# Performance work log

Measured on AMD Instinct MI355X. Metric: run time of the kernel, lower is better.

The kernel has to match this reference:

```python
import jax, jax.numpy as jnp
import numpy as np

B, N, H = 8, 2000, 64  # batch, num_nodes(=input_dim), hidden(num_gru_units)


def _laplacian_self_loop(a):
    # batched: norm = D^{-1/2} (A + I) D^{-1/2}
    m = a + jnp.eye(a.shape[-1], dtype=a.dtype)
    d_inv_sqrt = jnp.sum(m, axis=-1) ** -0.5  # (B, N)
    return d_inv_sqrt[..., :, None] * m * d_inv_sqrt[..., None, :]


def _graph_conv(inputs, hidden_flat, adj, windd, W2, b2, W3, b3, W, b, out_dim):
    b_, _, n = inputs.shape
    # dynamic wind-based adjacency
    wind_now = inputs[:, 2, :] * 360.0  # (B, N)
    direction = jnp.abs(windd[None, :, :] - wind_now[:, :, None])  # (B, N, N)
    direction = jnp.where(direction > 360.0, 180.0, direction)
    d1 = jnp.maximum(jnp.cos(direction * (jnp.pi / 180.0)), 0.0)
    a = d1 @ W2.T + b2 + (adj @ W3.T + b3)[None]  # (B, N, N)
    a1 = _laplacian_self_loop(jnp.maximum(a, 0.0))
    # graph conv: concat [x, h] then A @ [.] then Linear
    x = jnp.concatenate([inputs[:, 0, :, None], hidden_flat.reshape(b_, n, H)], axis=2)  # (B,N,H+1)
    y = jnp.einsum('bij,bjh->bih', a1, x) @ W.T + b  # (B, N, out_dim)
    return y.reshape(b_, n * out_dim)


def reference(inputs, hidden_state, adj, windd, W2, b2, W3, b3, W1a, b1a, W1b, b1b, Wca1, Wca2, Wsa):
    b_, _, n = inputs.shape
    conc = _graph_conv(inputs, hidden_state, adj, windd, W2, b2, W3, b3, W1a, b1a, 2 * H)
    conc = conc.reshape(b_, 2 * H, n)  # faithful reshape (input_dim == N)
    # --- channel attention (CBAM) ---
    avg = jnp.mean(conc, axis=2, keepdims=True)  # (B, 2H, 1)
    mx = jnp.max(conc, axis=2, keepdims=True)
    def fc(v):
        return jnp.einsum('oc,bcx->box', Wca2, jax.nn.relu(jnp.einsum('oc,bcx->box', Wca1, v)))
    ca = jax.nn.sigmoid(fc(avg) + fc(mx))  # (B, 2H, 1)
    conc = ca * conc
    # --- spatial attention ---
    s = jnp.stack([jnp.mean(conc, axis=1), jnp.max(conc, axis=1)], axis=1)  # (B, 2, N)
    sa = jax.lax.conv_general_dilated(s, Wsa, window_strides=(1,), padding=((3, 3),),
                                      dimension_numbers=('NCH', 'OIH', 'NCH'))  # (B,1,N)
    conc = jax.nn.sigmoid(sa) * conc
    # --- GRU gates ---
    conc = jax.nn.sigmoid(conc.reshape(b_, 2 * H * n))
    r, u = jnp.split(conc, 2, axis=1)  # each (B, N*H)
    c = jnp.tanh(_graph_conv(inputs, r * hidden_state, adj, windd, W2, b2, W3, b3, W1b, b1b, H))
    new_hidden_state = u * hidden_state + (1.0 - u) * c
    return new_hidden_state


def setup_inputs() -> dict:
    key = jax.random.key(0)
    ks = jax.random.split(key, 12)
    inputs = jax.random.uniform(ks[0], (B, 3, N), dtype=jnp.float32)
    hidden_state = jax.random.normal(ks[1], (B, N * H), dtype=jnp.float32) * 0.1
    adj = jax.random.uniform(ks[2], (N, N), dtype=jnp.float32)
    windd = jax.random.uniform(ks[3], (N, N), dtype=jnp.float32) * 360.0
    sN = 1.0 / np.sqrt(N)
    W2 = jax.random.normal(ks[4], (N, N), dtype=jnp.float32) * sN
    b2 = jnp.zeros((N,), jnp.float32)
    W3 = jax.random.normal(ks[5], (N, N), dtype=jnp.float32) * sN
    b3 = jnp.zeros((N,), jnp.float32)
    sI = 1.0 / np.sqrt(H + 1)
    W1a = jax.random.normal(ks[6], (2 * H, H + 1), dtype=jnp.float32) * sI
    b1a = jnp.ones((2 * H,), jnp.float32)  # bias=1.0 in graph_conv1
    W1b = jax.random.normal(ks[7], (H, H + 1), dtype=jnp.float32) * sI
    b1b = jnp.zeros((H,), jnp.float32)
    Wca1 = jax.random.normal(ks[8], (2 * H // 16, 2 * H), dtype=jnp.float32) * (1.0 / np.sqrt(2 * H))
    Wca2 = jax.random.normal(ks[9], (2 * H, 2 * H // 16), dtype=jnp.float32) * (1.0 / np.sqrt(2 * H // 16))
    Wsa = jax.random.normal(ks[10], (1, 2, 7), dtype=jnp.float32) * (1.0 / np.sqrt(14))
    return {'inputs': inputs, 'hidden_state': hidden_state, 'adj': adj, 'windd': windd,
            'W2': W2, 'b2': b2, 'W3': W3, 'b3': b3, 'W1a': W1a, 'b1a': b1a,
            'W1b': W1b, 'b1b': b1b, 'Wca1': Wca1, 'Wca2': Wca2, 'Wsa': Wsa}
```

## Files before the change

### kernel.cpp

```cpp
#include <hip/hip_runtime.h>

#define NN 2000
#define BB 8
#define P  2048
#define NIT 32

typedef __attribute__((ext_vector_type(8))) short bf16x8;
typedef __attribute__((ext_vector_type(4))) float f32x4;

__device__ __forceinline__ float sigf(float x) { return 1.0f / (1.0f + expf(-x)); }

__device__ __forceinline__ short f2bf(float x) {
    union { float f; unsigned u; } v; v.f = x;
    unsigned r = v.u + 0x7fffu + ((v.u >> 16) & 1u);
    return (short)(r >> 16);
}
__device__ __forceinline__ float bf2f(short h) {
    union { unsigned u; float f; } v; v.u = ((unsigned)(unsigned short)h) << 16; return v.f;
}

__device__ __forceinline__ void gl2lds16(const short* g, short* l) {
    __builtin_amdgcn_global_load_lds(
        (const __attribute__((address_space(1))) void*)g,
        (__attribute__((address_space(3))) void*)l, 16, 0, 0);
}

__global__ __launch_bounds__(256) void k_cvtW(
    const float* __restrict__ s0, const float* __restrict__ s1, const float* __restrict__ s2,
    short* __restrict__ d0, short* __restrict__ d1, short* __restrict__ d2)
{
    const int i = blockIdx.x, sel = blockIdx.y, t = threadIdx.x;
    const float* s = (sel == 0) ? s0 : (sel == 1) ? s1 : s2;
    short* d = ((sel == 0) ? d0 : (sel == 1) ? d1 : d2) + ((size_t)i) * P + t * 8;
    bf16x8 v;
#pragma unroll
    for (int e = 0; e < 8; ++e) v[e] = 0;
    if (i < NN && t < 250) {
        const float* p = s + (size_t)i * NN + t * 8;
        float4 x0 = *(const float4*)p;
        float4 x1 = *(const float4*)(p + 4);
        float a[8] = {x0.x,x0.y,x0.z,x0.w,x1.x,x1.y,x1.z,x1.w};
#pragma unroll
        for (int e = 0; e < 8; ++e) v[e] = f2bf(a[e]);
    }
    *(bf16x8*)d = v;
}

__global__ __launch_bounds__(256) void k_cvtD1(
    const float* __restrict__ windd, const float* __restrict__ inputs, short* __restrict__ d1bf)
{
    const int i = blockIdx.x, t = threadIdx.x;
    const bool live = (i < NN) && (t < 250);
    float a[8];
    if (live) {
        const float* p = windd + (size_t)i * NN + t * 8;
        float4 x0 = *(const float4*)p;
        float4 x1 = *(const float4*)(p + 4);
        a[0]=x0.x; a[1]=x0.y; a[2]=x0.z; a[3]=x0.w;
        a[4]=x1.x; a[5]=x1.y; a[6]=x1.z; a[7]=x1.w;
    }
#pragma unroll
    for (int b = 0; b < BB; ++b) {
        bf16x8 v;
#pragma unroll
        for (int e = 0; e < 8; ++e) v[e] = 0;
        if (live) {
            const float wn = inputs[(size_t)b * 3 * NN + 2 * NN + i] * 360.0f;
#pragma unroll
            for (int e = 0; e < 8; ++e) {
                float dd = fabsf(a[e] - wn);
                dd = (dd > 360.0f) ? 180.0f : dd;
                float c = __cosf(dd * 0.01745329251994329577f);
                v[e] = f2bf(fmaxf(c, 0.0f));
            }
        }
        *(bf16x8*)(d1bf + ((size_t)b * P + i) * P + t * 8) = v;
    }
}

__global__ __launch_bounds__(512, 2) void k_gd(
    const short* __restrict__ d1bf, const short* __restrict__ W2bf,
    const float* __restrict__ b2, const short* __restrict__ adjw,
    short* __restrict__ m_bf)
{
    __shared__ char smem[131072];
    const int t = threadIdx.x;
    const int w = t >> 6, lane = t & 63;
    const int wm = w >> 2, wn = w & 3;
    const int lr = lane & 15, lq = lane >> 4;
    const int tile = blockIdx.x;
    const int b = blockIdx.y;
    const int i0 = (tile & 7) * 256;
    const int j0 = (tile >> 3) * 256;
    const short* A  = d1bf + (size_t)b * P * P;
    const short* Bm = W2bf;

    const short* srcA[4];
    const short* srcB[4];
#pragma unroll
    for (int q = 0; q < 4; ++q) {
        const int c = q * 512 + t;
        const int r = c >> 3;
        const int g = (c & 7) ^ (r & 7);
        srcA[q] = A  + (size_t)(i0 + r) * P + g * 8;
        srcB[q] = Bm + (size_t)(j0 + r) * P + g * 8;
    }

#define STAGE_A(slot, ktI) do {                                                        \
        gl2lds16(srcA[0] + (ktI) * 64, (short*)(smem + (slot) * 32768 + (w * 64) * 16));          \
        gl2lds16(srcA[1] + (ktI) * 64, (short*)(smem + (slot) * 32768 + (512 + w * 64) * 16));    \
        gl2lds16(srcA[2] + (ktI) * 64, (short*)(smem + (slot) * 32768 + (1024 + w * 64) * 16));   \
        gl2lds16(srcA[3] + (ktI) * 64, (short*)(smem + (slot) * 32768 + (1536 + w * 64) * 16)); } while (0)
#define STAGE_B(slot, ktI) do {                                                        \
        gl2lds16(srcB[0] + (ktI) * 64, (short*)(smem + 65536 + (slot) * 32768 + (w * 64) * 16));          \
        gl2lds16(srcB[1] + (ktI) * 64, (short*)(smem + 65536 + (slot) * 32768 + (512 + w * 64) * 16));    \
        gl2lds16(srcB[2] + (ktI) * 64, (short*)(smem + 65536 + (slot) * 32768 + (1024 + w * 64) * 16));   \
        gl2lds16(srcB[3] + (ktI) * 64, (short*)(smem + 65536 + (slot) * 32768 + (1536 + w * 64) * 16)); } while (0)

    const int fx0 = (lq << 4) ^ ((lr & 7) << 4);
    const int fx1 = ((4 + lq) << 4) ^ ((lr & 7) << 4);
    const int arowB = (wm * 128 + lr) * 128;
    const int browB = (wn * 64 + lr) * 128;

    f32x4 acc[8][4];
#pragma unroll
    for (int m = 0; m < 8; ++m)
#pragma unroll
        for (int n = 0; n < 4; ++n) acc[m][n] = (f32x4){0.f, 0.f, 0.f, 0.f};
    bf16x8 aF[4][2], bF[4][2];

    STAGE_A(0, 0);
    STAGE_B(0, 0);
    asm volatile("s_waitcnt vmcnt(0)" ::: "memory");
    __builtin_amdgcn_s_barrier();
    asm volatile("" ::: "memory");

#define MFMA_(a_, b_, m, n) acc[m][n] = __builtin_amdgcn_mfma_f32_16x16x32_bf16(a_, b_, acc[m][n], 0, 0, 0)

    for (int kt = 0; kt < NIT; ++kt) {
        char* curA = smem + (kt & 1) * 32768;
        char* curB = smem + 65536 + (kt & 1) * 32768;
        const int stgSlot = (kt + 1) & 1;
        const int stgKt = (kt + 1 < NIT) ? (kt + 1) : (NIT - 1);

#pragma unroll
        for (int m = 0; m < 4; ++m) {
            aF[m][0] = *(const bf16x8*)(curA + arowB + m * 2048 + fx0);
            aF[m][1] = *(const bf16x8*)(curA + arowB + m * 2048 + fx1);
        }
#pragma unroll
        for (int n = 0; n < 4; ++n) {
            bF[n][0] = *(const bf16x8*)(curB + browB + n * 2048 + fx0);
            bF[n][1] = *(const bf16x8*)(curB + browB + n * 2048 + fx1);
        }
        STAGE_A(stgSlot, stgKt);
        asm volatile("s_waitcnt lgkmcnt(0)" ::: "memory");
        __builtin_amdgcn_sched_barrier(0);
        __builtin_amdgcn_s_setprio(1);
#pragma unroll
        for (int m = 0; m < 4; ++m)
#pragma unroll
            for (int n = 0; n < 4; ++n) {
                MFMA_(aF[m][0], bF[n][0], m, n);
                MFMA_(aF[m][1], bF[n][1], m, n);
            }
        __builtin_amdgcn_s_setprio(0);

#pragma unroll
        for (int m = 0; m < 4; ++m) {
            aF[m][0] = *(const bf16x8*)(curA + arowB + (m + 4) * 2048 + fx0);
            aF[m][1] = *(const bf16x8*)(curA + arowB + (m + 4) * 2048 + fx1);
        }
        STAGE_B(stgSlot, stgKt);
        asm volatile("s_waitcnt lgkmcnt(0)" ::: "memory");
        __builtin_amdgcn_sched_barrier(0);
        __builtin_amdgcn_s_setprio(1);
#pragma unroll
        for (int m = 0; m < 4; ++m)
#pragma unroll
            for (int n = 0; n < 4; ++n) {
                MFMA_(aF[m][0], bF[n][0], m + 4, n);
                MFMA_(aF[m][1], bF[n][1], m + 4, n);
            }
        __builtin_amdgcn_s_setprio(0);

        asm volatile("s_waitcnt vmcnt(0)" ::: "memory");
        __builtin_amdgcn_s_barrier();
        asm volatile("" ::: "memory");
    }

    const int rbase = i0 + wm * 128 + lq * 4;
    const int cbase = j0 + wn * 64 + lr;
#pragma unroll
    for (int m = 0; m < 8; ++m) {
#pragma unroll
        for (int n = 0; n < 4; ++n) {
            const int col = cbase + n * 16;
#pragma unroll
            for (int q = 0; q < 4; ++q) {
                const int row = rbase + m * 16 + q;
                short o = 0;
                if (row < NN && col < NN) {
                    float x = acc[m][n][q] + b2[col] + bf2f(adjw[(size_t)row * NN + col]);
                    x = fmaxf(x, 0.0f);
                    if (row == col) x += 1.0f;
                    o = f2bf(x);
                }
                m_bf[((size_t)b * P + row) * P + col] = o;
            }
        }
    }
#undef MFMA_
#undef STAGE_A
#undef STAGE_B
}

template<int EPI, int OUTD>
__global__ __launch_bounds__(256) void k_mfma(
    const short* __restrict__ Abase, const short* __restrict__ Bbase,
    const float* __restrict__ bias, const short* __restrict__ adjw,
    void* __restrict__ Cout, float* __restrict__ part, size_t aBatch)
{
    __shared__ short shA[4096];
    __shared__ short shB[4096];
    const int t = threadIdx.x;
    const int w = t >> 6, lane = t & 63;
    const int wr = w >> 1, wc = w & 1;

    int i0, j0, b, kt = 0;
    if (EPI == 2) {
        i0 = blockIdx.x * 128; j0 = 0; kt = blockIdx.y; b = blockIdx.z;
    } else {
        i0 = blockIdx.x * 128; j0 = blockIdx.y * 128; b = 0;
    }
    const int kb = (EPI == 2) ? kt * (P / 4) : 0;
    const int ke = (EPI == 2) ? kt * (P / 4) + (P / 4) : P;

    const short* A  = Abase + (size_t)b * aBatch;
    const short* Bm = Bbase + ((EPI == 2) ? (size_t)b * 128 * P : (size_t)0);

    f32x4 acc[4][4];
#pragma unroll
    for (int m = 0; m < 4; ++m)
#pragma unroll
        for (int n = 0; n < 4; ++n) acc[m][n] = (f32x4){0.f, 0.f, 0.f, 0.f};

    const int lidx0 = w * 128 + lane;
    const int lidx1 = lidx0 + 64;
    const short* aS0 = A  + (size_t)(i0 + (lidx0 >> 2)) * P + (lidx0 & 3) * 8;
    const short* aS1 = A  + (size_t)(i0 + (lidx1 >> 2)) * P + (lidx1 & 3) * 8;
    const short* bS0 = Bm + (size_t)(j0 + (lidx0 >> 2)) * P + (lidx0 & 3) * 8;
    const short* bS1 = Bm + (size_t)(j0 + (lidx1 >> 2)) * P + (lidx1 & 3) * 8;
    short* ldA0 = shA + (w * 128) * 8;
    short* ldA1 = shA + (w * 128 + 64) * 8;
    short* ldB0 = shB + (w * 128) * 8;
    short* ldB1 = shB + (w * 128 + 64) * 8;

    const int lr = lane & 15, lq = lane >> 4;
    const int aoff = (wr * 64 + lr) * 32 + lq * 8;
    const int boff = (wc * 64 + lr) * 32 + lq * 8;

    for (int k0 = kb; k0 < ke; k0 += 32) {
        gl2lds16(aS0 + k0, ldA0);
        gl2lds16(aS1 + k0, ldA1);
        gl2lds16(bS0 + k0, ldB0);
        gl2lds16(bS1 + k0, ldB1);
        __syncthreads();
        bf16x8 aF[4], bF[4];
#pragma unroll
        for (int m = 0; m < 4; ++m) aF[m] = *(const bf16x8*)(shA + aoff + m * 512);
#pragma unroll
        for (int n = 0; n < 4; ++n) bF[n] = *(const bf16x8*)(shB + boff + n * 512);
#pragma unroll
        for (int m = 0; m < 4; ++m)
#pragma unroll
            for (int n = 0; n < 4; ++n)
                acc[m][n] = __builtin_amdgcn_mfma_f32_16x16x32_bf16(aF[m], bF[n], acc[m][n], 0, 0, 0);
        __syncthreads();
    }

    const int rbase = i0 + wr * 64 + lq * 4;
    const int cbase = j0 + wc * 64 + lr;
#pragma unroll
    for (int m = 0; m < 4; ++m) {
#pragma unroll
        for (int n = 0; n < 4; ++n) {
            const int col = cbase + n * 16;
#pragma unroll
            for (int q = 0; q < 4; ++q) {
                const int row = rbase + m * 16 + q;
                float v = acc[m][n][q];
                if (EPI == 0) {
                    if (row < NN && col < NN)
                        ((short*)Cout)[(size_t)row * NN + col] = f2bf(v + bias[col]);
                } else {
                    if (row < NN && col < OUTD)
                        part[((size_t)(kt * BB + b) * NN + row) * OUTD + col] = v;
                }
            }
        }
    }
}

template<int OUTD>
__global__ __launch_bounds__(256) void k_comb(
    const float* __restrict__ part, const float* __restrict__ dinv,
    const float* __restrict__ bias, float* __restrict__ out)
{
    const size_t idx = (size_t)blockIdx.x * 256 + threadIdx.x;
    const size_t S = (size_t)BB * NN * OUTD;
    if (idx >= S) return;
    const int o = (int)(idx % OUTD);
    const size_t r = idx / OUTD;
    const int i = (int)(r % NN);
    const int b = (int)(r / NN);
    float s = ((part[idx] + part[idx + S]) + (part[idx + 2 * S] + part[idx + 3 * S]));
    out[idx] = s * dinv[b * NN + i] + bias[o];
}

__global__ __launch_bounds__(256) void k_rowsum_bf(const short* __restrict__ m_bf, float* __restrict__ dinv)
{
    const int i = blockIdx.x, b = blockIdx.y;
    const short* p = m_bf + ((size_t)b * P + i) * P + threadIdx.x * 8;
    bf16x8 v = *(const bf16x8*)p;
    float s = 0.0f;
#pragma unroll
    for (int e = 0; e < 8; ++e) s += bf2f(v[e]);
#pragma unroll
    for (int off = 32; off > 0; off >>= 1) s += __shfl_down(s, off);
    __shared__ float red[4];
    if ((threadIdx.x & 63) == 0) red[threadIdx.x >> 6] = s;
    __syncthreads();
    if (threadIdx.x == 0) dinv[b * NN + i] = rsqrtf(red[0] + red[1] + red[2] + red[3]);
}

template<int OUT>
__global__ __launch_bounds__(128) void k_xwT(
    const float* __restrict__ inputs, const float* __restrict__ hsrc,
    const float* __restrict__ W, const float* __restrict__ dinv, short* __restrict__ zT)
{
    const int b = blockIdx.y;
    const int j0 = blockIdx.x * 16;
    const int t = threadIdx.x;
    __shared__ float wl[128 * 65];
    __shared__ float xs[16 * 66];
    __shared__ float dj[16];
    for (int idx = t; idx < OUT * 65; idx += 128) wl[idx] = W[idx];
    for (int idx = t; idx < 16 * 64; idx += 128) {
        int jj = idx >> 6, hh = idx & 63, j = j0 + jj;
        xs[jj * 66 + 1 + hh] = (j < NN) ? hsrc[((size_t)b * NN + j) * 64 + hh] : 0.0f;
    }
    if (t < 16) {
        int j = j0 + t;
        xs[t * 66] = (j < NN) ? inputs[(size_t)b * 3 * NN + j] : 0.0f;
        dj[t] = (j < NN) ? dinv[b * NN + j] : 0.0f;
    }
    __syncthreads();
    for (int jj = 0; jj < 16; ++jj) {
        float a = 0.0f;
        if (t < OUT) {
            const float* xr = &xs[jj * 66];
            const float* wr = &wl[t * 65];
#pragma unroll
            for (int c = 0; c < 65; ++c) a = fmaf(xr[c], wr[c], a);
        }
        int j = j0 + jj;
        zT[((size_t)b * 128 + t) * P + j] = (t < OUT && j < NN) ? f2bf(a * dj[jj]) : (short)0;
    }
}

__global__ __launch_bounds__(256) void k_chred(const float* __restrict__ conc,
                                               float* __restrict__ avg, float* __restrict__ mx)
{
    const int bc = blockIdx.x;
    const float* p = conc + (size_t)bc * NN;
    float s = 0.0f, mv = -3.402823466e+38f;
    for (int n = threadIdx.x; n < NN; n += 256) { float v = p[n]; s += v; mv = fmaxf(mv, v); }
#pragma unroll
    for (int off = 32; off > 0; off >>= 1) {
        s += __shfl_down(s, off);
        mv = fmaxf(mv, __shfl_down(mv, off));
    }
    __shared__ float rs[4], rm[4];
    if ((threadIdx.x & 63) == 0) { rs[threadIdx.x >> 6] = s; rm[threadIdx.x >> 6] = mv; }
    __syncthreads();
    if (threadIdx.x == 0) {
        avg[bc] = (rs[0] + rs[1] + rs[2] + rs[3]) * (1.0f / NN);
        mx[bc]  = fmaxf(fmaxf(rm[0], rm[1]), fmaxf(rm[2], rm[3]));
    }
}

__global__ __launch_bounds__(128) void k_ca(
    const float* __restrict__ avg, const float* __restrict__ mx,
    const float* __restrict__ Wca1, const float* __restrict__ Wca2, float* __restrict__ ca)
{
    const int b = blockIdx.x, t = threadIdx.x;
    __shared__ float av[128], mv[128], h[16];
    av[t] = avg[b * 128 + t];
    mv[t] = mx[b * 128 + t];
    __syncthreads();
    if (t < 16) {
        int o8 = t & 7;
        const float* src = (t < 8) ? av : mv;
        float s = 0.0f;
        for (int c = 0; c < 128; ++c) s = fmaf(Wca1[o8 * 128 + c], src[c], s);
        h[t] = fmaxf(s, 0.0f);
    }
    __syncthreads();
    float s = 0.0f;
#pragma unroll
    for (int k = 0; k < 8; ++k) s = fmaf(Wca2[t * 8 + k], h[k] + h[8 + k], s);
    ca[b * 128 + t] = sigf(s);
}

__global__ __launch_bounds__(256) void k_satgate(
    const float* __restrict__ conc, const float* __restrict__ ca,
    const float* __restrict__ Wsa, const float* __restrict__ hidden,
    float* __restrict__ rh, float* __restrict__ u)
{
    const int b = blockIdx.y;
    const int n0 = blockIdx.x * 256;
    const int t = threadIdx.x;
    __shared__ float cas[128];
    __shared__ float wsa[14];
    __shared__ float s0l[262], s1l[262];
    if (t < 128) cas[t] = ca[b * 128 + t];
    if (t >= 128 && t < 142) wsa[t - 128] = Wsa[t - 128];
    __syncthreads();

    const float* cb = conc + (size_t)b * NN * 128;
    {
        const int n = n0 + t;
        float sm = 0.0f, sx = -3.402823466e+38f;
        if (n < NN) {
            for (int c = 0; c < 128; ++c) {
                float v = cas[c] * cb[(size_t)c * NN + n];
                sm += v; sx = fmaxf(sx, v);
            }
            s0l[t + 3] = sm * (1.0f / 128.0f);
            s1l[t + 3] = sx;
        } else { s0l[t + 3] = 0.0f; s1l[t + 3] = 0.0f; }
    }
    if (t < 6) {
        const int hn = (t < 3) ? (n0 - 3 + t) : (n0 + 256 + (t - 3));
        const int hi = (t < 3) ? t : (256 + t);
        float sm = 0.0f, sx = -3.402823466e+38f;
        if (hn >= 0 && hn < NN) {
            for (int c = 0; c < 128; ++c) {
                float v = cas[c] * cb[(size_t)c * NN + hn];
                sm += v; sx = fmaxf(sx, v);
            }
            s0l[hi] = sm * (1.0f / 128.0f);
            s1l[hi] = sx;
        } else { s0l[hi] = 0.0f; s1l[hi] = 0.0f; }
    }
    __syncthreads();

    const int n = n0 + t;
    if (n >= NN) return;
    float sa = 0.0f;
#pragma unroll
    for (int k = 0; k < 7; ++k)
        sa += wsa[k] * s0l[t + k] + wsa[7 + k] * s1l[t + k];
    float gs = sigf(sa);
    for (int c = 0; c < 128; ++c) {
        float v = gs * cas[c] * cb[(size_t)c * NN + n];
        float g = sigf(v);
        if (c < 64)
            rh[(size_t)b * NN * 64 + (size_t)c * NN + n] =
                g * hidden[(size_t)b * NN * 64 + (size_t)c * NN + n];
        else
            u[(size_t)b * NN * 64 + (size_t)(c - 64) * NN + n] = g;
    }
}

__global__ __launch_bounds__(256) void k_fin(
    const float* __restrict__ u, const float* __restrict__ hidden,
    const float* __restrict__ cpre, float* __restrict__ out)
{
    const size_t idx = (size_t)blockIdx.x * 256 + threadIdx.x;
    if (idx >= (size_t)BB * NN * 64) return;
    float uu = u[idx];
    out[idx] = uu * hidden[idx] + (1.0f - uu) * tanhf(cpre[idx]);
}

extern "C" void kernel_launch(void* const* d_in, const int* in_sizes, int n_in,
                              void* d_out, int out_size, void* d_ws, size_t ws_size,
                              hipStream_t stream)
{
    (void)in_sizes; (void)n_in; (void)out_size; (void)ws_size;
    const float* inputs = (const float*)d_in[0];
    const float* hidden = (const float*)d_in[1];
    const float* adj    = (const float*)d_in[2];
    const float* windd  = (const float*)d_in[3];
    const float* W2     = (const float*)d_in[4];
    const float* b2     = (const float*)d_in[5];
    const float* W3     = (const float*)d_in[6];
    const float* b3     = (const float*)d_in[7];
    const float* W1a    = (const float*)d_in[8];
    const float* b1a    = (const float*)d_in[9];
    const float* W1b    = (const float*)d_in[10];
    const float* b1b    = (const float*)d_in[11];
    const float* Wca1   = (const float*)d_in[12];
    const float* Wca2   = (const float*)d_in[13];
    const float* Wsa    = (const float*)d_in[14];
    float* out = (float*)d_out;

    char* W = (char*)d_ws;
    short* adjW3bf = (short*)(W + 0);
    short* W2bf    = (short*)(W + 8000000);
    short* W3bf    = (short*)(W + 16388608);
    short* adjbf   = (short*)(W + 24777216);
    short* m_bf    = (short*)(W + 16388608);
    char* D = W + 83497472;
    short* d1bf = (short*)D;
    float* dinv = (float*)(D + 0);
    float* avgb = (float*)(D + 64000);
    float* mxb  = (float*)(D + 68096);
    float* cab  = (float*)(D + 72192);
    short* zT   = (short*)(D + 204800);
    float* conc = (float*)(D + 4399104);
    float* rh   = (float*)(D + 12591104);
    float* ubuf = (float*)(D + 16687104);
    float* cpre = (float*)(D + 20783104);
    float* part = (float*)(D + 24879104);

    const size_t PP = (size_t)P * P;

    k_cvtW<<<dim3(P, 3), 256, 0, stream>>>(W2, W3, adj, W2bf, W3bf, adjbf);
    k_cvtD1<<<P, 256, 0, stream>>>(windd, inputs, d1bf);
    k_mfma<0, 0><<<dim3(16, 16, 1), 256, 0, stream>>>(adjbf, W3bf, b3, nullptr, adjW3bf, nullptr, 0);
    k_gd<<<dim3(64, BB), 512, 0, stream>>>(d1bf, W2bf, b2, adjW3bf, m_bf);
    k_rowsum_bf<<<dim3(NN, BB), 256, 0, stream>>>(m_bf, dinv);
    k_xwT<128><<<dim3(128, BB), 128, 0, stream>>>(inputs, hidden, W1a, dinv, zT);
    k_mfma<2, 128><<<dim3(16, 4, BB), 256, 0, stream>>>(m_bf, zT, nullptr, nullptr, nullptr, part, PP);
    k_comb<128><<<(BB * NN * 128 + 255) / 256, 256, 0, stream>>>(part, dinv, b1a, conc);
    k_chred<<<BB * 128, 256, 0, stream>>>(conc, avgb, mxb);
    k_ca<<<BB, 128, 0, stream>>>(avgb, mxb, Wca1, Wca2, cab);
    k_satgate<<<dim3(8, BB), 256, 0, stream>>>(conc, cab, Wsa, hidden, rh, ubuf);
    k_xwT<64><<<dim3(128, BB), 128, 0, stream>>>(inputs, rh, W1b, dinv, zT);
    k_mfma<2, 64><<<dim3(16, 4, BB), 256, 0, stream>>>(m_bf, zT, nullptr, nullptr, nullptr, part, PP);
    k_comb<64><<<(BB * NN * 64 + 255) / 256, 256, 0, stream>>>(part, dinv, b1b, cpre);
    k_fin<<<(BB * NN * 64 + 255) / 256, 256, 0, stream>>>(ubuf, hidden, cpre, out);
}
```

Baseline: 420.0 us.

## Issue all prefetch at loop top, store split-K partials as bf16, fuse final combine

The big GEMM kernel now issues the global-to-LDS prefetch for both A and B at the start of each k-iteration instead of interleaving it between the two MFMA halves. Split-K partial sums are written in bf16 rather than fp32, which halves that traffic but adds rounding error to the partials. The last combine kernel and the GRU final-blend kernel are merged into one, removing the cpre intermediate buffer and one launch.

```diff
diff --git a/kernel.cpp b/kernel.cpp
--- a/kernel.cpp
+++ b/kernel.cpp
@@ -106,12 +106,11 @@
         srcB[q] = Bm + (size_t)(j0 + r) * P + g * 8;
     }
 
-#define STAGE_A(slot, ktI) do {                                                        \
+#define STAGE_ALL(slot, ktI) do {                                                      \
         gl2lds16(srcA[0] + (ktI) * 64, (short*)(smem + (slot) * 32768 + (w * 64) * 16));          \
         gl2lds16(srcA[1] + (ktI) * 64, (short*)(smem + (slot) * 32768 + (512 + w * 64) * 16));    \
         gl2lds16(srcA[2] + (ktI) * 64, (short*)(smem + (slot) * 32768 + (1024 + w * 64) * 16));   \
-        gl2lds16(srcA[3] + (ktI) * 64, (short*)(smem + (slot) * 32768 + (1536 + w * 64) * 16)); } while (0)
-#define STAGE_B(slot, ktI) do {                                                        \
+        gl2lds16(srcA[3] + (ktI) * 64, (short*)(smem + (slot) * 32768 + (1536 + w * 64) * 16));   \
         gl2lds16(srcB[0] + (ktI) * 64, (short*)(smem + 65536 + (slot) * 32768 + (w * 64) * 16));          \
         gl2lds16(srcB[1] + (ktI) * 64, (short*)(smem + 65536 + (slot) * 32768 + (512 + w * 64) * 16));    \
         gl2lds16(srcB[2] + (ktI) * 64, (short*)(smem + 65536 + (slot) * 32768 + (1024 + w * 64) * 16));   \
@@ -129,8 +128,7 @@
         for (int n = 0; n < 4; ++n) acc[m][n] = (f32x4){0.f, 0.f, 0.f, 0.f};
     bf16x8 aF[4][2], bF[4][2];
 
-    STAGE_A(0, 0);
-    STAGE_B(0, 0);
+    STAGE_ALL(0, 0);
     asm volatile("s_waitcnt vmcnt(0)" ::: "memory");
     __builtin_amdgcn_s_barrier();
     asm volatile("" ::: "memory");
@@ -143,6 +141,8 @@
         const int stgSlot = (kt + 1) & 1;
         const int stgKt = (kt + 1 < NIT) ? (kt + 1) : (NIT - 1);
 
+        STAGE_ALL(stgSlot, stgKt);
+
 #pragma unroll
         for (int m = 0; m < 4; ++m) {
             aF[m][0] = *(const bf16x8*)(curA + arowB + m * 2048 + fx0);
@@ -153,7 +153,6 @@
             bF[n][0] = *(const bf16x8*)(curB + browB + n * 2048 + fx0);
             bF[n][1] = *(const bf16x8*)(curB + browB + n * 2048 + fx1);
         }
-        STAGE_A(stgSlot, stgKt);
         asm volatile("s_waitcnt lgkmcnt(0)" ::: "memory");
         __builtin_amdgcn_sched_barrier(0);
         __builtin_amdgcn_s_setprio(1);
@@ -171,7 +170,6 @@
             aF[m][0] = *(const bf16x8*)(curA + arowB + (m + 4) * 2048 + fx0);
             aF[m][1] = *(const bf16x8*)(curA + arowB + (m + 4) * 2048 + fx1);
         }
-        STAGE_B(stgSlot, stgKt);
         asm volatile("s_waitcnt lgkmcnt(0)" ::: "memory");
         __builtin_amdgcn_sched_barrier(0);
         __builtin_amdgcn_s_setprio(1);
@@ -211,15 +209,14 @@
         }
     }
 #undef MFMA_
-#undef STAGE_A
-#undef STAGE_B
+#undef STAGE_ALL
 }
 
 template<int EPI, int OUTD>
 __global__ __launch_bounds__(256) void k_mfma(
     const short* __restrict__ Abase, const short* __restrict__ Bbase,
     const float* __restrict__ bias, const short* __restrict__ adjw,
-    void* __restrict__ Cout, float* __restrict__ part, size_t aBatch)
+    void* __restrict__ Cout, short* __restrict__ part, size_t aBatch)
 {
     __shared__ short shA[4096];
     __shared__ short shB[4096];
@@ -295,7 +292,7 @@
                         ((short*)Cout)[(size_t)row * NN + col] = f2bf(v + bias[col]);
                 } else {
                     if (row < NN && col < OUTD)
-                        part[((size_t)(kt * BB + b) * NN + row) * OUTD + col] = v;
+                        part[((size_t)(kt * BB + b) * NN + row) * OUTD + col] = f2bf(v);
                 }
             }
         }
@@ -304,7 +301,7 @@
 
 template<int OUTD>
 __global__ __launch_bounds__(256) void k_comb(
-    const float* __restrict__ part, const float* __restrict__ dinv,
+    const short* __restrict__ part, const float* __restrict__ dinv,
     const float* __restrict__ bias, float* __restrict__ out)
 {
     const size_t idx = (size_t)blockIdx.x * 256 + threadIdx.x;
@@ -314,8 +311,28 @@
     const size_t r = idx / OUTD;
     const int i = (int)(r % NN);
     const int b = (int)(r / NN);
-    float s = ((part[idx] + part[idx + S]) + (part[idx + 2 * S] + part[idx + 3 * S]));
+    float s = (bf2f(part[idx]) + bf2f(part[idx + S])) +
+              (bf2f(part[idx + 2 * S]) + bf2f(part[idx + 3 * S]));
     out[idx] = s * dinv[b * NN + i] + bias[o];
+}
+
+__global__ __launch_bounds__(256) void k_cfin(
+    const short* __restrict__ part, const float* __restrict__ dinv,
+    const float* __restrict__ bias, const float* __restrict__ u,
+    const float* __restrict__ hidden, float* __restrict__ out)
+{
+    const size_t idx = (size_t)blockIdx.x * 256 + threadIdx.x;
+    const size_t S = (size_t)BB * NN * 64;
+    if (idx >= S) return;
+    const int o = (int)(idx & 63);
+    const size_t r = idx >> 6;
+    const int i = (int)(r % NN);
+    const int b = (int)(r / NN);
+    float s = (bf2f(part[idx]) + bf2f(part[idx + S])) +
+              (bf2f(part[idx + 2 * S]) + bf2f(part[idx + 3 * S]));
+    float c = tanhf(s * dinv[b * NN + i] + bias[o]);
+    float uu = u[idx];
+    out[idx] = uu * hidden[idx] + (1.0f - uu) * c;
 }
 
 __global__ __launch_bounds__(256) void k_rowsum_bf(const short* __restrict__ m_bf, float* __restrict__ dinv)
@@ -472,16 +489,6 @@
         else
             u[(size_t)b * NN * 64 + (size_t)(c - 64) * NN + n] = g;
     }
-}
-
-__global__ __launch_bounds__(256) void k_fin(
-    const float* __restrict__ u, const float* __restrict__ hidden,
-    const float* __restrict__ cpre, float* __restrict__ out)
-{
-    const size_t idx = (size_t)blockIdx.x * 256 + threadIdx.x;
-    if (idx >= (size_t)BB * NN * 64) return;
-    float uu = u[idx];
-    out[idx] = uu * hidden[idx] + (1.0f - uu) * tanhf(cpre[idx]);
 }
 
 extern "C" void kernel_launch(void* const* d_in, const int* in_sizes, int n_in,
@@ -522,8 +529,7 @@
     float* conc = (float*)(D + 4399104);
     float* rh   = (float*)(D + 12591104);
     float* ubuf = (float*)(D + 16687104);
-    float* cpre = (float*)(D + 20783104);
-    float* part = (float*)(D + 24879104);
+    short* part = (short*)(D + 24879104);
 
     const size_t PP = (size_t)P * P;
 
@@ -540,6 +546,5 @@
     k_satgate<<<dim3(8, BB), 256, 0, stream>>>(conc, cab, Wsa, hidden, rh, ubuf);
     k_xwT<64><<<dim3(128, BB), 128, 0, stream>>>(inputs, rh, W1b, dinv, zT);
     k_mfma<2, 64><<<dim3(16, 4, BB), 256, 0, stream>>>(m_bf, zT, nullptr, nullptr, nullptr, part, PP);
-    k_comb<64><<<(BB * NN * 64 + 255) / 256, 256, 0, stream>>>(part, dinv, b1b, cpre);
-    k_fin<<<(BB * NN * 64 + 255) / 256, 256, 0, stream>>>(ubuf, hidden, cpre, out);
-}
+    k_cfin<<<(BB * NN * 64 + 255) / 256, 256, 0, stream>>>(part, dinv, b1b, ubuf, hidden, out);
+}
```

Result: no change. 411.9 us (-1.9%).
